# Kernel optimization log

Measured on AMD Instinct MI355X. Metric: run time of the kernel, lower is better.

## Reference

```python
import jax, jax.numpy as jnp
import numpy as np

B, N, T, OBS, ACT, M, EMB = 128, 128, 256, 512, 64, 16, 128
H = T // 2  # bi-LSTM hidden per direction
EPS = 1e-5


def _ln(x, g, b):
    mu = x.mean(-1, keepdims=True)
    var = ((x - mu) ** 2).mean(-1, keepdims=True)
    return (x - mu) / jnp.sqrt(var + EPS) * g + b


def _lstm_dir(xs, Wih, Whh, bih, bhh):
    # xs: [m, T] -> hidden states [m, H]; torch gate order i,f,g,o
    h0 = jnp.zeros(xs.shape[:-2] + (H,), xs.dtype)

    def cell(carry, x):
        h, c = carry
        z = x @ Wih.T + h @ Whh.T + bih + bhh
        i, f, g, o = jnp.split(z, 4, axis=-1)
        c = jax.nn.sigmoid(f) * c + jax.nn.sigmoid(i) * jnp.tanh(g)
        h = jax.nn.sigmoid(o) * jnp.tanh(c)
        return (h, c), h

    (_, _), hs = jax.lax.scan(cell, (h0, h0), xs)
    return hs


def setup_inputs() -> dict:
    key = jax.random.key(0)
    ks = iter(jax.random.split(key, 32))

    def lin(fi, shape):
        return jax.random.normal(next(ks), shape, jnp.float32) / float(np.sqrt(fi))

    z = lambda *s: jnp.zeros(s, jnp.float32)
    o = lambda *s: jnp.ones(s, jnp.float32)
    return dict(
        obs=jax.random.normal(next(ks), (B, N, OBS), jnp.float32),
        W1=lin(OBS, (OBS, T)), b1=z(T), g1=o(T), be1=z(T),
        W2=lin(T, (T, T)), b2=z(T), g2=o(T), be2=z(T),
        Wa1=lin(T, (T, EMB)), ba1=z(EMB),
        Wa2=lin(EMB, (EMB, EMB)), ba2=z(EMB),
        Wa3=lin(EMB, (EMB, 1)), ba3=z(1),
        Wf_ih=lin(T, (4 * H, T)), Wf_hh=lin(H, (4 * H, H)), bf_ih=z(4 * H), bf_hh=z(4 * H),
        Wb_ih=lin(T, (4 * H, T)), Wb_hh=lin(H, (4 * H, H)), bb_ih=z(4 * H), bb_hh=z(4 * H),
        W3=lin(T, (T, T)), b3=z(T), g3=o(T), be3=z(T),
        W4=lin(T, (T, ACT)), b4=z(ACT), g4=o(ACT), be4=z(ACT),
    )


def reference(obs, W1, b1, g1, be1, W2, b2, g2, be2,
              Wa1, ba1, Wa2, ba2, Wa3, ba3,
              Wf_ih, Wf_hh, bf_ih, bf_hh, Wb_ih, Wb_hh, bb_ih, bb_hh,
              W3, b3, g3, be3, W4, b4, g4, be4):
    # actor_1: Linear -> LN -> ReLU -> Linear -> LN
    h = jax.nn.relu(_ln(obs @ W1 + b1, g1, be1))
    thoughts = _ln(h @ W2 + b2, g2, be2)              # [B,N,T]

    # attention unit: 2-layer MLP + sigmoid
    a = jax.nn.relu(thoughts @ Wa1 + ba1)
    a = jax.nn.relu(a @ Wa2 + ba2)
    init_prob = jax.nn.sigmoid(a @ Wa3 + ba3)          # [B,N,1]
    is_init = init_prob[..., 0] > 0.4                  # [B,N]

    # pairwise squared distances via bmm (same expansion as torch code)
    dot = jnp.einsum('bit,bjt->bij', thoughts, thoughts)
    sq = jnp.diagonal(dot, axis1=1, axis2=2)           # [B,N]
    dists = sq[:, None, :] - 2.0 * dot + sq[:, :, None]

    # top-m nearest neighbors per agent, then agent-index order (matches j-loop order)
    _, idx = jax.lax.top_k(-dists, M)                  # [B,N,M]
    idx = jnp.sort(idx, axis=-1)

    bidx = jnp.arange(B)[:, None, None]
    aidx = jnp.arange(N)[None, :, None]
    C = jnp.zeros((B, N, N), thoughts.dtype).at[bidx, aidx, idx].set(1.0)
    C = C * is_init[..., None].astype(thoughts.dtype)

    old_thoughts = thoughts

    # sequential per-agent communication: gather group, bi-LSTM, scatter back
    def update_one(th, grp_idx, flags):
        def step(t, inp):
            gi, fl = inp
            grp = t[gi]                                 # [M,T]
            hf = _lstm_dir(grp, Wf_ih, Wf_hh, bf_ih, bf_hh)
            hb = _lstm_dir(grp[::-1], Wb_ih, Wb_hh, bb_ih, bb_hh)[::-1]
            integ = jnp.concatenate([hf, hb], -1)       # [M,T]
            t = t.at[gi].set(jnp.where(fl, integ, grp))
            return t, None
        t, _ = jax.lax.scan(step, th, (grp_idx, flags))
        return t

    new_thoughts = jax.vmap(update_one)(thoughts, idx, is_init)

    # actor_2: ReLU -> Linear -> LN -> Linear -> LN -> Tanh
    h2 = jax.nn.relu(new_thoughts)
    h2 = _ln(h2 @ W3 + b3, g3, be3)
    acts = jnp.tanh(_ln(h2 @ W4 + b4, g4, be4))
    return acts, C, init_prob, is_init, new_thoughts, old_thoughts
```

## Files before the change

### kernel.cpp

```cpp
#include <hip/hip_runtime.h>
#include <math.h>

typedef __attribute__((ext_vector_type(8))) short bf16x8;
typedef __attribute__((ext_vector_type(4))) float f32x4;

__device__ __forceinline__ unsigned short f2bf(float x) {
    unsigned int u = __float_as_uint(x);
    u += 0x7fffu + ((u >> 16) & 1u);
    return (unsigned short)(u >> 16);
}
__device__ __forceinline__ float bf2f(unsigned short b) {
    return __uint_as_float(((unsigned int)b) << 16);
}
__device__ __forceinline__ float fsig(float z) {
    float e = __expf(-z);
    return __builtin_amdgcn_rcpf(1.f + e);
}
__device__ __forceinline__ float ftanh(float x) {
    float e = __expf(-2.f * x);
    float s = __builtin_amdgcn_rcpf(1.f + e);
    return fmaf(2.f, s, -1.f);
}
__device__ __forceinline__ bf16x8 pack8(float4 a, float4 b) {
    bf16x8 r;
    r[0] = (short)f2bf(a.x); r[1] = (short)f2bf(a.y);
    r[2] = (short)f2bf(a.z); r[3] = (short)f2bf(a.w);
    r[4] = (short)f2bf(b.x); r[5] = (short)f2bf(b.y);
    r[6] = (short)f2bf(b.z); r[7] = (short)f2bf(b.w);
    return r;
}

__global__ void prep_kernel(const float* __restrict__ Wf_ih, const float* __restrict__ Wb_ih,
                            const float* __restrict__ Wf_hh, const float* __restrict__ Wb_hh,
                            const float* __restrict__ bf_ih, const float* __restrict__ bf_hh,
                            const float* __restrict__ bb_ih, const float* __restrict__ bb_hh,
                            unsigned short* __restrict__ wihbf,
                            unsigned short* __restrict__ whhbf,
                            float* __restrict__ biasz) {
    int i = blockIdx.x * 256 + threadIdx.x;
    if (i < 131072) {
        wihbf[i]          = f2bf(Wf_ih[i]);
        wihbf[131072 + i] = f2bf(Wb_ih[i]);
    }
    if (i < 65536) {
        whhbf[i]         = f2bf(Wf_hh[i]);
        whhbf[65536 + i] = f2bf(Wb_hh[i]);
    }
    if (i < 512) {
        biasz[i]       = bf_ih[i] + bf_hh[i];
        biasz[512 + i] = bb_ih[i] + bb_hh[i];
    }
}

__global__ __launch_bounds__(256) void gemm64(const float* __restrict__ A,
                                              const float* __restrict__ Bm,
                                              const float* __restrict__ bias,
                                              float* __restrict__ C,
                                              int M, int N, int K, int flags) {
    __shared__ float As[16][68];
    __shared__ float Bs[16][68];
    const int t = threadIdx.x;
    const int row0 = blockIdx.y * 64, col0 = blockIdx.x * 64;
    const int tm = t >> 4, tn = t & 15;
    float acc[4][4] = {};
    for (int k0 = 0; k0 < K; k0 += 16) {
        {
            int r = t >> 2, kq = (t & 3) * 4;
            float4 v = *(const float4*)(A + (size_t)(row0 + r) * K + k0 + kq);
            if (flags & 2) {
                v.x = fmaxf(v.x, 0.f); v.y = fmaxf(v.y, 0.f);
                v.z = fmaxf(v.z, 0.f); v.w = fmaxf(v.w, 0.f);
            }
            As[kq + 0][r] = v.x; As[kq + 1][r] = v.y;
            As[kq + 2][r] = v.z; As[kq + 3][r] = v.w;
        }
        {
            int kk = t >> 4, nq = (t & 15) * 4;
            float4 v = *(const float4*)(Bm + (size_t)(k0 + kk) * N + col0 + nq);
            *(float4*)&Bs[kk][nq] = v;
        }
        __syncthreads();
#pragma unroll
        for (int kk = 0; kk < 16; ++kk) {
            float a[4], b[4];
#pragma unroll
            for (int i = 0; i < 4; ++i) a[i] = As[kk][tm * 4 + i];
#pragma unroll
            for (int j = 0; j < 4; ++j) b[j] = Bs[kk][tn * 4 + j];
#pragma unroll
            for (int i = 0; i < 4; ++i)
#pragma unroll
                for (int j = 0; j < 4; ++j) acc[i][j] = fmaf(a[i], b[j], acc[i][j]);
        }
        __syncthreads();
    }
#pragma unroll
    for (int i = 0; i < 4; ++i) {
#pragma unroll
        for (int j = 0; j < 4; ++j) {
            int col = col0 + tn * 4 + j;
            float v = acc[i][j] + (bias ? bias[col] : 0.f);
            if (flags & 1) v = fmaxf(v, 0.f);
            C[(size_t)(row0 + tm * 4 + i) * N + col] = v;
        }
    }
}

__global__ __launch_bounds__(256) void ln256_kernel(const float* __restrict__ X,
                                                    float* __restrict__ Y,
                                                    float* __restrict__ Y2,
                                                    const float* __restrict__ gam,
                                                    const float* __restrict__ bet,
                                                    int relu) {
#pragma clang fp contract(off)
    int row = blockIdx.x * 4 + (threadIdx.x >> 6);
    int l = threadIdx.x & 63;
    float4 x = *(const float4*)(X + (size_t)row * 256 + l * 4);
    float s = x.x + x.y + x.z + x.w;
#pragma unroll
    for (int d = 1; d < 64; d <<= 1) s += __shfl_xor(s, d);
    float mu = s * (1.f / 256.f);
    float d0 = x.x - mu, d1 = x.y - mu, d2 = x.z - mu, d3 = x.w - mu;
    float ss = d0 * d0 + d1 * d1 + d2 * d2 + d3 * d3;
#pragma unroll
    for (int d = 1; d < 64; d <<= 1) ss += __shfl_xor(ss, d);
    float var = ss * (1.f / 256.f);
    float sd = sqrtf(var + 1e-5f);
    float4 y;
    y.x = (d0 / sd) * gam[l * 4 + 0] + bet[l * 4 + 0];
    y.y = (d1 / sd) * gam[l * 4 + 1] + bet[l * 4 + 1];
    y.z = (d2 / sd) * gam[l * 4 + 2] + bet[l * 4 + 2];
    y.w = (d3 / sd) * gam[l * 4 + 3] + bet[l * 4 + 3];
    if (relu) {
        y.x = fmaxf(y.x, 0.f); y.y = fmaxf(y.y, 0.f);
        y.z = fmaxf(y.z, 0.f); y.w = fmaxf(y.w, 0.f);
    }
    *(float4*)(Y + (size_t)row * 256 + l * 4) = y;
    if (Y2) *(float4*)(Y2 + (size_t)row * 256 + l * 4) = y;
}

__global__ __launch_bounds__(256) void ln64_tanh_kernel(const float* __restrict__ X,
                                                        float* __restrict__ Y,
                                                        const float* __restrict__ gam,
                                                        const float* __restrict__ bet) {
#pragma clang fp contract(off)
    int row = blockIdx.x * 4 + (threadIdx.x >> 6);
    int l = threadIdx.x & 63;
    float x = X[(size_t)row * 64 + l];
    float s = x;
#pragma unroll
    for (int d = 1; d < 64; d <<= 1) s += __shfl_xor(s, d);
    float mu = s * (1.f / 64.f);
    float dx = x - mu;
    float ss = dx * dx;
#pragma unroll
    for (int d = 1; d < 64; d <<= 1) ss += __shfl_xor(ss, d);
    float var = ss * (1.f / 64.f);
    float sd = sqrtf(var + 1e-5f);
    float y = tanhf((dx / sd) * gam[l] + bet[l]);
    Y[(size_t)row * 64 + l] = y;
}

__global__ __launch_bounds__(256) void attn_head_kernel(const float* __restrict__ a2,
                                                        const float* __restrict__ Wa3,
                                                        const float* __restrict__ ba3,
                                                        float* __restrict__ outP,
                                                        float* __restrict__ outInit,
                                                        int* __restrict__ flags) {
#pragma clang fp contract(off)
    int row = blockIdx.x * 4 + (threadIdx.x >> 6);
    int l = threadIdx.x & 63;
    float s = a2[(size_t)row * 128 + l] * Wa3[l] + a2[(size_t)row * 128 + 64 + l] * Wa3[64 + l];
#pragma unroll
    for (int d = 1; d < 64; d <<= 1) s += __shfl_xor(s, d);
    s += ba3[0];
    float p = 1.f / (1.f + expf(-s));
    if (l == 0) {
        outP[row] = p;
        int f = (p > 0.4f) ? 1 : 0;
        outInit[row] = f ? 1.f : 0.f;
        flags[row] = f;
    }
}

__global__ __launch_bounds__(256) void dot_kernel(const float* __restrict__ th,
                                                  float* __restrict__ dotm) {
    __shared__ float As[16][68];
    __shared__ float Bs[16][132];
    const int b = blockIdx.x >> 1, half = blockIdx.x & 1;
    const int t = threadIdx.x;
    const int tm = t >> 4, tn = t & 15;
    float acc[4][8] = {};
    const float* base = th + (size_t)b * 128 * 256;
    for (int k0 = 0; k0 < 256; k0 += 16) {
        {
            int r = t >> 2, kq = (t & 3) * 4;
            float4 v = *(const float4*)(base + (size_t)(half * 64 + r) * 256 + k0 + kq);
            As[kq + 0][r] = v.x; As[kq + 1][r] = v.y;
            As[kq + 2][r] = v.z; As[kq + 3][r] = v.w;
        }
        {
            int n = t >> 1, kq = (t & 1) * 8;
            const float* src = base + (size_t)n * 256 + k0 + kq;
            float4 v0 = *(const float4*)src;
            float4 v1 = *(const float4*)(src + 4);
            Bs[kq + 0][n] = v0.x; Bs[kq + 1][n] = v0.y;
            Bs[kq + 2][n] = v0.z; Bs[kq + 3][n] = v0.w;
            Bs[kq + 4][n] = v1.x; Bs[kq + 5][n] = v1.y;
            Bs[kq + 6][n] = v1.z; Bs[kq + 7][n] = v1.w;
        }
        __syncthreads();
#pragma unroll
        for (int kk = 0; kk < 16; ++kk) {
            float a[4], bb[8];
#pragma unroll
            for (int i = 0; i < 4; ++i) a[i] = As[kk][tm * 4 + i];
#pragma unroll
            for (int j = 0; j < 8; ++j) bb[j] = Bs[kk][tn * 8 + j];
#pragma unroll
            for (int i = 0; i < 4; ++i)
#pragma unroll
                for (int j = 0; j < 8; ++j) acc[i][j] = fmaf(a[i], bb[j], acc[i][j]);
        }
        __syncthreads();
    }
#pragma unroll
    for (int i = 0; i < 4; ++i)
#pragma unroll
        for (int j = 0; j < 8; ++j)
            dotm[(size_t)b * 16384 + (size_t)(half * 64 + tm * 4 + i) * 128 + tn * 8 + j] = acc[i][j];
}

__global__ void sq_kernel(const float* __restrict__ dotm, float* __restrict__ sq) {
    int i = blockIdx.x * 256 + threadIdx.x;
    int b = i >> 7, n = i & 127;
    sq[i] = dotm[(size_t)b * 16384 + (size_t)n * 129];
}

__global__ __launch_bounds__(256) void topk_kernel(const float* __restrict__ dotm,
                                                   const float* __restrict__ sq,
                                                   const int* __restrict__ flags,
                                                   float* __restrict__ outC,
                                                   int* __restrict__ idxb) {
#pragma clang fp contract(off)
    int row = blockIdx.x * 4 + (threadIdx.x >> 6);
    int l = threadIdx.x & 63;
    int b = row >> 7;
    const float* drow = dotm + (size_t)row * 128;
    float sqi = sq[row];
    float t0 = 2.f * drow[l];
    float v0 = sq[b * 128 + l] - t0; v0 = v0 + sqi;
    float t1 = 2.f * drow[64 + l];
    float v1 = sq[b * 128 + 64 + l] - t1; v1 = v1 + sqi;

    unsigned long long mlo = 0ull, mhi = 0ull;
#pragma unroll 1
    for (int n = 0; n < 16; ++n) {
        float bv = v0; int bi = l;
        if (v1 < bv) { bv = v1; bi = 64 + l; }
#pragma unroll
        for (int d = 1; d < 64; d <<= 1) {
            float ov = __shfl_xor(bv, d);
            int oi = __shfl_xor(bi, d);
            if (ov < bv || (ov == bv && oi < bi)) { bv = ov; bi = oi; }
        }
        if (bi < 64) mlo |= (1ull << bi); else mhi |= (1ull << (bi - 64));
        if (l == bi) v0 = __builtin_inff();
        if (64 + l == bi) v1 = __builtin_inff();
    }
    float fl = (flags[row] != 0) ? 1.f : 0.f;
    outC[(size_t)row * 128 + l]      = fl * (((mlo >> l) & 1ull) ? 1.f : 0.f);
    outC[(size_t)row * 128 + 64 + l] = fl * (((mhi >> l) & 1ull) ? 1.f : 0.f);
    if (l < 16) {
        int cnt = 0, found = -1;
        for (int jj = 0; jj < 128; ++jj) {
            bool bit = (jj < 64) ? ((mlo >> jj) & 1ull) : ((mhi >> (jj - 64)) & 1ull);
            if (bit) { if (cnt == l) { found = jj; break; } ++cnt; }
        }
        idxb[(size_t)row * 16 + l] = found;
    }
}

__global__ __launch_bounds__(512, 2) void chain_kernel(float* __restrict__ th,
                                                       const unsigned short* __restrict__ whhbf,
                                                       const unsigned short* __restrict__ wihbf,
                                                       const float* __restrict__ biasz,
                                                       const int* __restrict__ idxb,
                                                       const int* __restrict__ flags) {
    const int b = blockIdx.x;
    const int t = threadIdx.x;
    const int l = t & 63, lr = l & 15, lg = l >> 4;
    const int w = t >> 6, dir = w >> 2, wd = w & 3;

    __shared__ __align__(16) unsigned short thl[128 * 256];
    __shared__ __align__(16) unsigned short xgs2[2 * 4 * 16 * 16 * 8];
    __shared__ __align__(16) unsigned short hsnap[2][18][128];
    __shared__ int idxl[2048];
    __shared__ int flg[128];

    {
        int r = t >> 2, c0 = (t & 3) * 64;
        const float* src = th + (size_t)(b * 128 + r) * 256 + c0;
        char* rowb = (char*)thl + r * 512;
        int swz = (r & 7) << 4;
#pragma unroll
        for (int i = 0; i < 8; ++i) {
            float4 v0 = *(const float4*)(src + i * 8);
            float4 v1 = *(const float4*)(src + i * 8 + 4);
            *(bf16x8*)(rowb + (((c0 + i * 8) * 2) ^ swz)) = pack8(v0, v1);
        }
    }
    if (t < 128) flg[t] = flags[b * 128 + t];
    if (t < 256) {
        int d2 = t >> 7, j = t & 127;
        hsnap[d2][0][j] = 0;
        hsnap[d2][17][j] = 0;
    }
#pragma unroll
    for (int c = 0; c < 4; ++c) idxl[t + c * 512] = idxb[(size_t)b * 2048 + c * 512 + t];

    bf16x8 wf[4][2][4];
    {
        const unsigned short* whh = whhbf + (size_t)dir * 65536;
#pragma unroll
        for (int G = 0; G < 4; ++G)
#pragma unroll
            for (int hf = 0; hf < 2; ++hf) {
                int gate = G * 128 + wd * 32 + 2 * lr + hf;
#pragma unroll
                for (int kc = 0; kc < 4; ++kc)
                    wf[G][hf][kc] = *(const bf16x8*)(whh + (size_t)gate * 128 + kc * 32 + lg * 8);
            }
    }
    const unsigned short* wih = wihbf + (size_t)dir * 131072;
    float bzr[8];
#pragma unroll
    for (int tt = 0; tt < 8; ++tt)
        bzr[tt] = biasz[dir * 512 + (tt >> 1) * 128 + wd * 32 + 2 * lr + (tt & 1)];
    __syncthreads();

    const int xgbase = ((dir * 4 + wd) * 16) * 16 * 8;

    for (int ag = 0; ag < 128; ++ag) {
        if (!flg[ag]) continue;
        const int gi_lr = idxl[ag * 16 + lr];

        {
            f32x4 xa[8];
#pragma unroll
            for (int tt = 0; tt < 8; ++tt)
                xa[tt] = (f32x4){bzr[tt], bzr[tt], bzr[tt], bzr[tt]};
            const char* arow = (const char*)thl + gi_lr * 512;
            const int aswz = (gi_lr & 7) << 4;
#pragma unroll
            for (int kc = 0; kc < 8; ++kc) {
                bf16x8 af = *(const bf16x8*)(arow + ((kc * 64 + lg * 16) ^ aswz));
#pragma unroll
                for (int tt = 0; tt < 8; ++tt) {
                    const unsigned short* wb =
                        wih + (size_t)((tt >> 1) * 128 + wd * 32 + 2 * lr + (tt & 1)) * 256 +
                        kc * 32 + lg * 8;
                    xa[tt] = __builtin_amdgcn_mfma_f32_16x16x32_bf16(
                        af, *(const bf16x8*)wb, xa[tt], 0, 0, 0);
                }
            }
#pragma unroll
            for (int r = 0; r < 4; ++r) {
                bf16x8 pk;
#pragma unroll
                for (int tt = 0; tt < 8; ++tt) pk[tt] = (short)f2bf(xa[tt][r]);
                int m = lg * 4 + r;
                *(bf16x8*)&xgs2[xgbase + (m * 16 + lr) * 8] = pk;
            }
        }
        __syncthreads();

        bf16x8 xpn = *(const bf16x8*)&xgs2[xgbase + ((dir ? 15 : 0) * 16 + lr) * 8];

        float cst0 = 0.f, cst1 = 0.f;
#pragma unroll
        for (int s = 0; s < 16; ++s) {
            const int m = dir ? (15 - s) : s;
            const int rprev = dir ? (m + 2) : m;
            bf16x8 xp = xpn;
            f32x4 acc[4][2];
#pragma unroll
            for (int G = 0; G < 4; ++G)
#pragma unroll
                for (int hf = 0; hf < 2; ++hf) {
                    float xv = bf2f((unsigned short)xp[G * 2 + hf]);
                    acc[G][hf] = (f32x4){xv, xv, xv, xv};
                }
#pragma unroll
            for (int kc = 0; kc < 4; ++kc) {
                bf16x8 ha = *(const bf16x8*)(&hsnap[dir][rprev][kc * 32 + lg * 8]);
#pragma unroll
                for (int G = 0; G < 4; ++G) {
                    acc[G][0] = __builtin_amdgcn_mfma_f32_16x16x32_bf16(
                        ha, wf[G][0][kc], acc[G][0], 0, 0, 0);
                    acc[G][1] = __builtin_amdgcn_mfma_f32_16x16x32_bf16(
                        ha, wf[G][1][kc], acc[G][1], 0, 0, 0);
                }
            }
            float i0 = fsig(acc[0][0][0]), f0 = fsig(acc[1][0][0]);
            float g0 = ftanh(acc[2][0][0]), o0 = fsig(acc[3][0][0]);
            cst0 = f0 * cst0 + i0 * g0;
            float h0 = o0 * ftanh(cst0);
            float i1 = fsig(acc[0][1][0]), f1 = fsig(acc[1][1][0]);
            float g1 = ftanh(acc[2][1][0]), o1 = fsig(acc[3][1][0]);
            cst1 = f1 * cst1 + i1 * g1;
            float h1 = o1 * ftanh(cst1);
            if (lg == 0) {
                unsigned int hw = (unsigned int)f2bf(h0) | ((unsigned int)f2bf(h1) << 16);
                *(unsigned int*)&hsnap[dir][m + 1][wd * 32 + 2 * lr] = hw;
            }
            if (s < 15) {
                int mn = dir ? (14 - s) : (s + 1);
                xpn = *(const bf16x8*)&xgs2[xgbase + (mn * 16 + lr) * 8];
            }
            __syncthreads();
        }

        {
            int d2 = t >> 8, m = (t >> 4) & 15, c8 = (t & 15) * 8;
            bf16x8 v = *(const bf16x8*)&hsnap[d2][m + 1][c8];
            int row = idxl[ag * 16 + m];
            *(bf16x8*)((char*)thl + row * 512 + (((d2 * 128 + c8) * 2) ^ ((row & 7) << 4))) = v;
        }
        __syncthreads();
    }

    {
        int r = t >> 2, c0 = (t & 3) * 64;
        const char* rowb = (const char*)thl + r * 512;
        int swz = (r & 7) << 4;
        float* dst = th + (size_t)(b * 128 + r) * 256 + c0;
#pragma unroll
        for (int i = 0; i < 8; ++i) {
            bf16x8 sv = *(const bf16x8*)(rowb + (((c0 + i * 8) * 2) ^ swz));
            float4 v0, v1;
            v0.x = bf2f((unsigned short)sv[0]); v0.y = bf2f((unsigned short)sv[1]);
            v0.z = bf2f((unsigned short)sv[2]); v0.w = bf2f((unsigned short)sv[3]);
            v1.x = bf2f((unsigned short)sv[4]); v1.y = bf2f((unsigned short)sv[5]);
            v1.z = bf2f((unsigned short)sv[6]); v1.w = bf2f((unsigned short)sv[7]);
            *(float4*)(dst + i * 8) = v0;
            *(float4*)(dst + i * 8 + 4) = v1;
        }
    }
}

extern "C" void kernel_launch(void* const* d_in, const int* in_sizes, int n_in,
                              void* d_out, int out_size, void* d_ws, size_t ws_size,
                              hipStream_t stream) {
    const float* obs  = (const float*)d_in[0];
    const float* W1   = (const float*)d_in[1];
    const float* b1   = (const float*)d_in[2];
    const float* gg1  = (const float*)d_in[3];
    const float* be1  = (const float*)d_in[4];
    const float* W2   = (const float*)d_in[5];
    const float* b2   = (const float*)d_in[6];
    const float* gg2  = (const float*)d_in[7];
    const float* be2  = (const float*)d_in[8];
    const float* Wa1  = (const float*)d_in[9];
    const float* ba1  = (const float*)d_in[10];
    const float* Wa2  = (const float*)d_in[11];
    const float* ba2  = (const float*)d_in[12];
    const float* Wa3  = (const float*)d_in[13];
    const float* ba3  = (const float*)d_in[14];
    const float* Wf_ih = (const float*)d_in[15];
    const float* Wf_hh = (const float*)d_in[16];
    const float* bf_ih = (const float*)d_in[17];
    const float* bf_hh = (const float*)d_in[18];
    const float* Wb_ih = (const float*)d_in[19];
    const float* Wb_hh = (const float*)d_in[20];
    const float* bb_ih = (const float*)d_in[21];
    const float* bb_hh = (const float*)d_in[22];
    const float* W3   = (const float*)d_in[23];
    const float* b3   = (const float*)d_in[24];
    const float* gg3  = (const float*)d_in[25];
    const float* be3  = (const float*)d_in[26];
    const float* W4   = (const float*)d_in[27];
    const float* b4   = (const float*)d_in[28];
    const float* gg4  = (const float*)d_in[29];
    const float* be4  = (const float*)d_in[30];

    float* out     = (float*)d_out;
    float* out_acts = out;
    float* out_C    = out + 1048576;
    float* out_ip   = out + 3145728;
    float* out_ii   = out + 3162112;
    float* out_nt   = out + 3178496;
    float* out_ot   = out + 7372800;

    float* ws    = (float*)d_ws;
    float* h1    = ws;
    float* abuf  = ws + 4194304;
    float* a2buf = ws + 6291456;
    unsigned short* wihbf = (unsigned short*)(ws + 8388608);
    float* biasz = ws + 8519680;
    unsigned short* whhbf = (unsigned short*)(ws + 8520704);
    float* sqb   = ws + 8586240;
    int* idxb    = (int*)(ws + 8602624);
    int* flagsb  = (int*)(ws + 8864768);

    prep_kernel<<<512, 256, 0, stream>>>(Wf_ih, Wb_ih, Wf_hh, Wb_hh,
                                         bf_ih, bf_hh, bb_ih, bb_hh,
                                         wihbf, whhbf, biasz);

    gemm64<<<dim3(4, 256), 256, 0, stream>>>(obs, W1, b1, h1, 16384, 256, 512, 0);
    ln256_kernel<<<4096, 256, 0, stream>>>(h1, h1, nullptr, gg1, be1, 1);
    gemm64<<<dim3(4, 256), 256, 0, stream>>>(h1, W2, b2, out_nt, 16384, 256, 256, 0);
    ln256_kernel<<<4096, 256, 0, stream>>>(out_nt, out_nt, out_ot, gg2, be2, 0);

    gemm64<<<dim3(2, 256), 256, 0, stream>>>(out_nt, Wa1, ba1, abuf, 16384, 128, 256, 1);
    gemm64<<<dim3(2, 256), 256, 0, stream>>>(abuf, Wa2, ba2, a2buf, 16384, 128, 128, 1);
    attn_head_kernel<<<4096, 256, 0, stream>>>(a2buf, Wa3, ba3, out_ip, out_ii, flagsb);

    dot_kernel<<<256, 256, 0, stream>>>(out_nt, abuf);
    sq_kernel<<<64, 256, 0, stream>>>(abuf, sqb);
    topk_kernel<<<4096, 256, 0, stream>>>(abuf, sqb, flagsb, out_C, idxb);

    chain_kernel<<<128, 512, 0, stream>>>(out_nt, whhbf, wihbf, biasz, idxb, flagsb);

    gemm64<<<dim3(4, 256), 256, 0, stream>>>(out_nt, W3, b3, h1, 16384, 256, 256, 2);
    ln256_kernel<<<4096, 256, 0, stream>>>(h1, h1, nullptr, gg3, be3, 0);
    gemm64<<<dim3(1, 256), 256, 0, stream>>>(h1, W4, b4, a2buf, 16384, 64, 256, 0);
    ln64_tanh_kernel<<<4096, 256, 0, stream>>>(a2buf, out_acts, gg4, be4);
}
```

Before: 4.000 ms.

## Halve chain kernel block to 256 threads with 64 gates per wave

The bi-LSTM chain kernel now runs 4 waves per block instead of 8. Each wave covers 64 hidden units per gate and keeps twice as many Whh fragments in registers. The gate-column mapping changes from interleaved pairs to contiguous 16-wide groups. The input projection is now added after the recurrent MFMAs instead of seeding the accumulator. The aim is to make each per-step __syncthreads cheaper, since fewer waves take part, and to give each wave more independent MFMAs. In exchange, the block has half the wave-level parallelism and much higher register pressure (64 bf16x8 weight fragments plus 64 accumulators), which could cause spills.

```diff
diff --git a/kernel.cpp b/kernel.cpp
--- a/kernel.cpp
+++ b/kernel.cpp
@@ -281,7 +281,7 @@
     }
 }
 
-__global__ __launch_bounds__(512, 2) void chain_kernel(float* __restrict__ th,
+__global__ __launch_bounds__(256, 1) void chain_kernel(float* __restrict__ th,
                                                        const unsigned short* __restrict__ whhbf,
                                                        const unsigned short* __restrict__ wihbf,
                                                        const float* __restrict__ biasz,
@@ -290,153 +290,172 @@
     const int b = blockIdx.x;
     const int t = threadIdx.x;
     const int l = t & 63, lr = l & 15, lg = l >> 4;
-    const int w = t >> 6, dir = w >> 2, wd = w & 3;
+    const int w = t >> 6, dir = w >> 1, ww = w & 1;
 
     __shared__ __align__(16) unsigned short thl[128 * 256];
-    __shared__ __align__(16) unsigned short xgs2[2 * 4 * 16 * 16 * 8];
+    __shared__ __align__(16) unsigned short xgs3[2 * 2 * 16 * 256];
     __shared__ __align__(16) unsigned short hsnap[2][18][128];
     __shared__ int idxl[2048];
     __shared__ int flg[128];
 
     {
-        int r = t >> 2, c0 = (t & 3) * 64;
+        int r = t >> 1, c0 = (t & 1) * 128;
         const float* src = th + (size_t)(b * 128 + r) * 256 + c0;
         char* rowb = (char*)thl + r * 512;
         int swz = (r & 7) << 4;
 #pragma unroll
-        for (int i = 0; i < 8; ++i) {
+        for (int i = 0; i < 16; ++i) {
             float4 v0 = *(const float4*)(src + i * 8);
             float4 v1 = *(const float4*)(src + i * 8 + 4);
             *(bf16x8*)(rowb + (((c0 + i * 8) * 2) ^ swz)) = pack8(v0, v1);
         }
     }
     if (t < 128) flg[t] = flags[b * 128 + t];
-    if (t < 256) {
+    {
         int d2 = t >> 7, j = t & 127;
         hsnap[d2][0][j] = 0;
         hsnap[d2][17][j] = 0;
     }
 #pragma unroll
-    for (int c = 0; c < 4; ++c) idxl[t + c * 512] = idxb[(size_t)b * 2048 + c * 512 + t];
-
-    bf16x8 wf[4][2][4];
+    for (int c = 0; c < 8; ++c) idxl[t + c * 256] = idxb[(size_t)b * 2048 + c * 256 + t];
+
+    bf16x8 wf[4][4][4];
     {
         const unsigned short* whh = whhbf + (size_t)dir * 65536;
 #pragma unroll
         for (int G = 0; G < 4; ++G)
 #pragma unroll
-            for (int hf = 0; hf < 2; ++hf) {
-                int gate = G * 128 + wd * 32 + 2 * lr + hf;
+            for (int q = 0; q < 4; ++q) {
+                int gate = G * 128 + ww * 64 + q * 16 + lr;
 #pragma unroll
                 for (int kc = 0; kc < 4; ++kc)
-                    wf[G][hf][kc] = *(const bf16x8*)(whh + (size_t)gate * 128 + kc * 32 + lg * 8);
+                    wf[G][q][kc] = *(const bf16x8*)(whh + (size_t)gate * 128 + kc * 32 + lg * 8);
             }
     }
     const unsigned short* wih = wihbf + (size_t)dir * 131072;
-    float bzr[8];
-#pragma unroll
-    for (int tt = 0; tt < 8; ++tt)
-        bzr[tt] = biasz[dir * 512 + (tt >> 1) * 128 + wd * 32 + 2 * lr + (tt & 1)];
+    float bzr[16];
+#pragma unroll
+    for (int G = 0; G < 4; ++G)
+#pragma unroll
+        for (int q = 0; q < 4; ++q)
+            bzr[G * 4 + q] = biasz[dir * 512 + G * 128 + ww * 64 + q * 16 + lr];
     __syncthreads();
 
-    const int xgbase = ((dir * 4 + wd) * 16) * 16 * 8;
+    const int xgbase = (dir * 2 + ww) * 16 * 256;
 
     for (int ag = 0; ag < 128; ++ag) {
         if (!flg[ag]) continue;
         const int gi_lr = idxl[ag * 16 + lr];
 
         {
-            f32x4 xa[8];
-#pragma unroll
-            for (int tt = 0; tt < 8; ++tt)
-                xa[tt] = (f32x4){bzr[tt], bzr[tt], bzr[tt], bzr[tt]};
+            f32x4 xa[4][4];
+#pragma unroll
+            for (int G = 0; G < 4; ++G)
+#pragma unroll
+                for (int q = 0; q < 4; ++q) {
+                    float bb = bzr[G * 4 + q];
+                    xa[G][q] = (f32x4){bb, bb, bb, bb};
+                }
             const char* arow = (const char*)thl + gi_lr * 512;
             const int aswz = (gi_lr & 7) << 4;
 #pragma unroll
             for (int kc = 0; kc < 8; ++kc) {
                 bf16x8 af = *(const bf16x8*)(arow + ((kc * 64 + lg * 16) ^ aswz));
 #pragma unroll
-                for (int tt = 0; tt < 8; ++tt) {
-                    const unsigned short* wb =
-                        wih + (size_t)((tt >> 1) * 128 + wd * 32 + 2 * lr + (tt & 1)) * 256 +
-                        kc * 32 + lg * 8;
-                    xa[tt] = __builtin_amdgcn_mfma_f32_16x16x32_bf16(
-                        af, *(const bf16x8*)wb, xa[tt], 0, 0, 0);
+                for (int G = 0; G < 4; ++G)
+#pragma unroll
+                    for (int q = 0; q < 4; ++q) {
+                        const unsigned short* wb =
+                            wih + (size_t)(G * 128 + ww * 64 + q * 16 + lr) * 256 +
+                            kc * 32 + lg * 8;
+                        xa[G][q] = __builtin_amdgcn_mfma_f32_16x16x32_bf16(
+                            af, *(const bf16x8*)wb, xa[G][q], 0, 0, 0);
+                    }
+            }
+#pragma unroll
+            for (int r = 0; r < 4; ++r) {
+                bf16x8 p0, p1;
+#pragma unroll
+                for (int q = 0; q < 4; ++q) {
+                    p0[q]     = (short)f2bf(xa[0][q][r]);
+                    p0[4 + q] = (short)f2bf(xa[1][q][r]);
+                    p1[q]     = (short)f2bf(xa[2][q][r]);
+                    p1[4 + q] = (short)f2bf(xa[3][q][r]);
                 }
-            }
-#pragma unroll
-            for (int r = 0; r < 4; ++r) {
-                bf16x8 pk;
-#pragma unroll
-                for (int tt = 0; tt < 8; ++tt) pk[tt] = (short)f2bf(xa[tt][r]);
                 int m = lg * 4 + r;
-                *(bf16x8*)&xgs2[xgbase + (m * 16 + lr) * 8] = pk;
+                unsigned short* dst = &xgs3[xgbase + m * 256 + lr * 16];
+                *(bf16x8*)dst = p0;
+                *(bf16x8*)(dst + 8) = p1;
             }
         }
         __syncthreads();
 
-        bf16x8 xpn = *(const bf16x8*)&xgs2[xgbase + ((dir ? 15 : 0) * 16 + lr) * 8];
-
-        float cst0 = 0.f, cst1 = 0.f;
-#pragma unroll
+        const int m0 = dir ? 15 : 0;
+        bf16x8 xq0 = *(const bf16x8*)&xgs3[xgbase + m0 * 256 + lr * 16];
+        bf16x8 xq1 = *(const bf16x8*)&xgs3[xgbase + m0 * 256 + lr * 16 + 8];
+
+        float cst[4] = {0.f, 0.f, 0.f, 0.f};
         for (int s = 0; s < 16; ++s) {
             const int m = dir ? (15 - s) : s;
             const int rprev = dir ? (m + 2) : m;
-            bf16x8 xp = xpn;
-            f32x4 acc[4][2];
+            f32x4 acc[4][4];
 #pragma unroll
             for (int G = 0; G < 4; ++G)
 #pragma unroll
-                for (int hf = 0; hf < 2; ++hf) {
-                    float xv = bf2f((unsigned short)xp[G * 2 + hf]);
-                    acc[G][hf] = (f32x4){xv, xv, xv, xv};
-                }
+                for (int q = 0; q < 4; ++q) acc[G][q] = (f32x4){0.f, 0.f, 0.f, 0.f};
 #pragma unroll
             for (int kc = 0; kc < 4; ++kc) {
                 bf16x8 ha = *(const bf16x8*)(&hsnap[dir][rprev][kc * 32 + lg * 8]);
 #pragma unroll
-                for (int G = 0; G < 4; ++G) {
-                    acc[G][0] = __builtin_amdgcn_mfma_f32_16x16x32_bf16(
-                        ha, wf[G][0][kc], acc[G][0], 0, 0, 0);
-                    acc[G][1] = __builtin_amdgcn_mfma_f32_16x16x32_bf16(
-                        ha, wf[G][1][kc], acc[G][1], 0, 0, 0);
-                }
-            }
-            float i0 = fsig(acc[0][0][0]), f0 = fsig(acc[1][0][0]);
-            float g0 = ftanh(acc[2][0][0]), o0 = fsig(acc[3][0][0]);
-            cst0 = f0 * cst0 + i0 * g0;
-            float h0 = o0 * ftanh(cst0);
-            float i1 = fsig(acc[0][1][0]), f1 = fsig(acc[1][1][0]);
-            float g1 = ftanh(acc[2][1][0]), o1 = fsig(acc[3][1][0]);
-            cst1 = f1 * cst1 + i1 * g1;
-            float h1 = o1 * ftanh(cst1);
-            if (lg == 0) {
-                unsigned int hw = (unsigned int)f2bf(h0) | ((unsigned int)f2bf(h1) << 16);
-                *(unsigned int*)&hsnap[dir][m + 1][wd * 32 + 2 * lr] = hw;
-            }
+                for (int G = 0; G < 4; ++G)
+#pragma unroll
+                    for (int q = 0; q < 4; ++q)
+                        acc[G][q] = __builtin_amdgcn_mfma_f32_16x16x32_bf16(
+                            ha, wf[G][q][kc], acc[G][q], 0, 0, 0);
+            }
+            bf16x8 x0 = xq0, x1 = xq1;
+            float hq[4];
+#pragma unroll
+            for (int q = 0; q < 4; ++q) {
+                float zi = acc[0][q][0] + bf2f((unsigned short)x0[q]);
+                float zf = acc[1][q][0] + bf2f((unsigned short)x0[4 + q]);
+                float zg = acc[2][q][0] + bf2f((unsigned short)x1[q]);
+                float zo = acc[3][q][0] + bf2f((unsigned short)x1[4 + q]);
+                float ig = fsig(zi), fg = fsig(zf), gv = ftanh(zg), og = fsig(zo);
+                cst[q] = fg * cst[q] + ig * gv;
+                hq[q] = og * ftanh(cst[q]);
+            }
+            float hsel = (lg == 0) ? hq[0] : (lg == 1) ? hq[1] : (lg == 2) ? hq[2] : hq[3];
+            hsnap[dir][m + 1][ww * 64 + lg * 16 + lr] = f2bf(hsel);
             if (s < 15) {
                 int mn = dir ? (14 - s) : (s + 1);
-                xpn = *(const bf16x8*)&xgs2[xgbase + (mn * 16 + lr) * 8];
+                xq0 = *(const bf16x8*)&xgs3[xgbase + mn * 256 + lr * 16];
+                xq1 = *(const bf16x8*)&xgs3[xgbase + mn * 256 + lr * 16 + 8];
             }
             __syncthreads();
         }
 
         {
-            int d2 = t >> 8, m = (t >> 4) & 15, c8 = (t & 15) * 8;
-            bf16x8 v = *(const bf16x8*)&hsnap[d2][m + 1][c8];
-            int row = idxl[ag * 16 + m];
-            *(bf16x8*)((char*)thl + row * 512 + (((d2 * 128 + c8) * 2) ^ ((row & 7) << 4))) = v;
+#pragma unroll
+            for (int i = 0; i < 2; ++i) {
+                int item = t + i * 256;
+                int d2 = item >> 8, m = (item >> 4) & 15, c8 = (item & 15) * 8;
+                bf16x8 v = *(const bf16x8*)&hsnap[d2][m + 1][c8];
+                int row = idxl[ag * 16 + m];
+                *(bf16x8*)((char*)thl + row * 512 +
+                           (((d2 * 128 + c8) * 2) ^ ((row & 7) << 4))) = v;
+            }
         }
         __syncthreads();
     }
 
     {
-        int r = t >> 2, c0 = (t & 3) * 64;
+        int r = t >> 1, c0 = (t & 1) * 128;
         const char* rowb = (const char*)thl + r * 512;
         int swz = (r & 7) << 4;
         float* dst = th + (size_t)(b * 128 + r) * 256 + c0;
 #pragma unroll
-        for (int i = 0; i < 8; ++i) {
+        for (int i = 0; i < 16; ++i) {
             bf16x8 sv = *(const bf16x8*)(rowb + (((c0 + i * 8) * 2) ^ swz));
             float4 v0, v1;
             v0.x = bf2f((unsigned short)sv[0]); v0.y = bf2f((unsigned short)sv[1]);
@@ -520,7 +539,7 @@
     sq_kernel<<<64, 256, 0, stream>>>(abuf, sqb);
     topk_kernel<<<4096, 256, 0, stream>>>(abuf, sqb, flagsb, out_C, idxb);
 
-    chain_kernel<<<128, 512, 0, stream>>>(out_nt, whhbf, wihbf, biasz, idxb, flagsb);
+    chain_kernel<<<128, 256, 0, stream>>>(out_nt, whhbf, wihbf, biasz, idxb, flagsb);
 
     gemm64<<<dim3(4, 256), 256, 0, stream>>>(out_nt, W3, b3, h1, 16384, 256, 256, 2);
     ln256_kernel<<<4096, 256, 0, stream>>>(h1, h1, nullptr, gg3, be3, 0);
```

New measurement: 4.582 ms. +14.6%, slower.
